# Kernel tuning notes

Measured on AMD Instinct MI355X. Metric: run time of the kernel, lower is better.

The kernel has to match this reference:

```python
import jax, jax.numpy as jnp
import numpy as np

B, C, H, W = 32, 3, 224, 224
P = 14            # n_patches per side
PS = H // P       # 16
D = 768           # embed_size
NH = 12           # heads
DH = D // NH      # 64
L = 12            # n_blocks
FF = 4 * D
OUT = 1000
S = P * P + 1     # 197 tokens


def positional_encoding(seq_len, d):
    i = jnp.arange(seq_len, dtype=jnp.float32)[:, None]
    j = jnp.arange(d, dtype=jnp.float32)[None, :]
    je = jnp.where(j % 2 == 0, j, j - 1)
    ang = i / jnp.power(10000.0, je / d)
    return jnp.where(j % 2 == 0, jnp.sin(ang), jnp.cos(ang))


def layernorm(x, g, b, eps=1e-5):
    mu = jnp.mean(x, axis=-1, keepdims=True)
    var = jnp.var(x, axis=-1, keepdims=True)
    return (x - mu) * jax.lax.rsqrt(var + eps) * g + b


def setup_inputs() -> dict:
    key = jax.random.key(0)
    ks = jax.random.split(key, 20)
    s = 0.02
    inp = {
        'images': jax.random.normal(ks[0], (B, C, H, W), jnp.float32),
        'W_patch': jax.random.normal(ks[1], (D, C * PS * PS), jnp.float32) * s,
        'b_patch': jnp.zeros((D,), jnp.float32),
        'class_token': jax.random.uniform(ks[2], (1, D), jnp.float32),
        'ln1_g': jnp.ones((L, D), jnp.float32),
        'ln1_b': jnp.zeros((L, D), jnp.float32),
        'Wq': jax.random.normal(ks[3], (L, NH, DH, DH), jnp.float32) * s,
        'bq': jnp.zeros((L, NH, DH), jnp.float32),
        'Wk': jax.random.normal(ks[4], (L, NH, DH, DH), jnp.float32) * s,
        'bk': jnp.zeros((L, NH, DH), jnp.float32),
        'Wv': jax.random.normal(ks[5], (L, NH, DH, DH), jnp.float32) * s,
        'bv': jnp.zeros((L, NH, DH), jnp.float32),
        'ln2_g': jnp.ones((L, D), jnp.float32),
        'ln2_b': jnp.zeros((L, D), jnp.float32),
        'W1': jax.random.normal(ks[6], (L, FF, D), jnp.float32) * s,
        'b1': jnp.zeros((L, FF), jnp.float32),
        'W2': jax.random.normal(ks[7], (L, D, FF), jnp.float32) * s,
        'b2': jnp.zeros((L, D), jnp.float32),
        'Wo': jax.random.normal(ks[8], (OUT, D), jnp.float32) * s,
        'bo': jnp.zeros((OUT,), jnp.float32),
    }
    return inp


def reference(images, W_patch, b_patch, class_token, ln1_g, ln1_b,
              Wq, bq, Wk, bk, Wv, bv, ln2_g, ln2_b, W1, b1, W2, b2, Wo, bo):
    b = images.shape[0]
    # patch extraction: [B,C,P,ps,P,ps] -> [B,P*P, C*ps*ps] (flatten order C,h,w)
    patches = images.reshape(b, C, P, PS, P, PS).transpose(0, 2, 4, 1, 3, 5)
    patches = patches.reshape(b, P * P, C * PS * PS)
    tokens = patches @ W_patch.T + b_patch                     # [B, P^2, D]
    cls = jnp.broadcast_to(class_token[None], (b, 1, D))
    x = jnp.concatenate([cls, tokens], axis=1)                 # [B, S, D]
    x = x + positional_encoding(S, D)

    scale = 1.0 / jnp.sqrt(jnp.float32(DH))
    for l in range(L):
        h = layernorm(x, ln1_g[l], ln1_b[l])
        hh = h.reshape(b, S, NH, DH)
        q = jnp.einsum('bshd,hed->bshe', hh, Wq[l]) + bq[l]
        k = jnp.einsum('bshd,hed->bshe', hh, Wk[l]) + bk[l]
        v = jnp.einsum('bshd,hed->bshe', hh, Wv[l]) + bv[l]
        scores = jnp.einsum('bshe,bthe->bhst', q, k) * scale   # [B,H,S,S]
        attn = jax.nn.softmax(scores, axis=-1)
        o = jnp.einsum('bhst,bthe->bshe', attn, v).reshape(b, S, D)
        x = x + o
        h2 = layernorm(x, ln2_g[l], ln2_b[l])
        ff = jax.nn.gelu(h2 @ W1[l].T + b1[l], approximate=False) @ W2[l].T + b2[l]
        x = x + ff

    logits = x[:, 0] @ Wo.T + bo                               # [B, OUT]
    return jax.nn.softmax(logits, axis=-1)
```

## Files before the change

### kernel.cpp

```cpp
#include <hip/hip_runtime.h>
#include <math.h>

static constexpr int kB   = 32;
static constexpr int kC   = 3;
static constexpr int kH   = 224;
static constexpr int kW   = 224;
static constexpr int kP   = 14;
static constexpr int kPS  = 16;
static constexpr int kD   = 768;
static constexpr int kNH  = 12;
static constexpr int kDH  = 64;
static constexpr int kL   = 12;
static constexpr int kFF  = 3072;
static constexpr int kOUT = 1000;
static constexpr int kS   = 197;
static constexpr int kTOK = kB * kS;
static constexpr int kNP  = kP * kP;
static constexpr int kMP  = 6400;
static constexpr int kQKV = 3 * kD;

typedef unsigned short u16;
typedef __attribute__((ext_vector_type(4))) float f32x4;
typedef __attribute__((ext_vector_type(8))) short bf16x8;

__device__ __forceinline__ u16 f2bf(float x) {
    unsigned u = __float_as_uint(x);
    return (u16)((u + 0x7FFFu + ((u >> 16) & 1u)) >> 16);
}
__device__ __forceinline__ float bf2f(u16 x) {
    return __uint_as_float((unsigned)x << 16);
}
__device__ __forceinline__ void cp16_async(void* lds, const void* g) {
    __builtin_amdgcn_global_load_lds((const __attribute__((address_space(1))) unsigned*)g,
                                     (__attribute__((address_space(3))) unsigned*)lds,
                                     16, 0, 0);
}

__global__ void vit_posenc(float* __restrict__ pos) {
    int idx = blockIdx.x * 256 + threadIdx.x;
    if (idx >= kS * kD) return;
    int s = idx / kD, d = idx % kD;
    int je = d & ~1;
    double p = pow(10000.0, (double)je / (double)kD);
    float ang = (float)((double)s / p);
    pos[idx] = (d & 1) ? cosf(ang) : sinf(ang);
}

__global__ void vit_im2col_bf16(const float* __restrict__ img, u16* __restrict__ patches) {
    long idx = (long)blockIdx.x * 256 + threadIdx.x;
    if (idx >= (long)kMP * kD) return;
    int col = (int)(idx % kD);
    long rp = idx / kD;
    if (rp >= (long)kB * kNP) { patches[idx] = 0; return; }
    int p = (int)(rp % kNP), b = (int)(rp / kNP);
    int c = col >> 8;
    int rem = col & 255;
    int i = rem >> 4, j = rem & 15;
    int py = p / kP, px = p % kP;
    patches[idx] = f2bf(img[(((long)b * kC + c) * kH + py * kPS + i) * kW + px * kPS + j]);
}

__global__ void vit_assemble(const float* __restrict__ tokens, const float* __restrict__ cls,
                             const float* __restrict__ pos, float* __restrict__ x) {
    long idx = (long)blockIdx.x * 256 + threadIdx.x;
    if (idx >= (long)kMP * kD) return;
    int d = (int)(idx % kD);
    long bs = idx / kD;
    if (bs >= kTOK) { x[idx] = 0.0f; return; }
    int s = (int)(bs % kS);
    long b = bs / kS;
    float v = (s == 0) ? cls[d] : tokens[((long)b * kNP + (s - 1)) * kD + d];
    x[idx] = v + pos[s * kD + d];
}

__global__ void cast_bf16(const float* __restrict__ in, u16* __restrict__ out, long n4) {
    long i = (long)blockIdx.x * 256 + threadIdx.x;
    if (i >= n4) return;
    float4 v = *(const float4*)(in + i * 4);
    *(ushort4*)(out + i * 4) = make_ushort4(f2bf(v.x), f2bf(v.y), f2bf(v.z), f2bf(v.w));
}

__global__ void zero_u16(u16* __restrict__ p, long n) {
    long i = (long)blockIdx.x * 256 + threadIdx.x;
    if (i < n) p[i] = 0;
}

__global__ void build_whb(const float* __restrict__ Wq, const float* __restrict__ Wk,
                          const float* __restrict__ Wv, const float* __restrict__ bq,
                          const float* __restrict__ bk, const float* __restrict__ bv,
                          u16* __restrict__ Wh, float* __restrict__ bh) {
    int idx = blockIdx.x * 256 + threadIdx.x;
    if (idx >= kNH * 192 * 64) return;
    int d = idx & 63;
    int r = (idx >> 6) % 192;
    int h = idx / (192 * 64);
    int sec = r >> 6, e = r & 63;
    const float* W = (sec == 0) ? Wq : (sec == 1) ? Wk : Wv;
    Wh[idx] = f2bf(W[((h << 6) + e) * 64 + d]);
    if (d == 0) {
        const float* bs = (sec == 0) ? bq : (sec == 1) ? bk : bv;
        bh[h * 192 + r] = bs[(h << 6) + e];
    }
}

__global__ __launch_bounds__(256) void vit_ln(const float* __restrict__ x,
                                              const float* __restrict__ g,
                                              const float* __restrict__ b,
                                              u16* __restrict__ out) {
    long t = blockIdx.x;
    const float* xr = x + t * kD;
    int tid = threadIdx.x;
    float v0 = xr[tid], v1 = xr[tid + 256], v2 = xr[tid + 512];
    float s  = v0 + v1 + v2;
    float sq = v0 * v0 + v1 * v1 + v2 * v2;
    #pragma unroll
    for (int o = 32; o; o >>= 1) { s += __shfl_xor(s, o); sq += __shfl_xor(sq, o); }
    __shared__ float red[8];
    int wid = tid >> 6, lane = tid & 63;
    if (lane == 0) { red[wid] = s; red[4 + wid] = sq; }
    __syncthreads();
    s  = red[0] + red[1] + red[2] + red[3];
    sq = red[4] + red[5] + red[6] + red[7];
    float mu  = s * (1.0f / kD);
    float var = sq * (1.0f / kD) - mu * mu;
    float rs  = rsqrtf(var + 1e-5f);
    u16* orow = out + t * kD;
    orow[tid]       = f2bf((v0 - mu) * rs * g[tid]       + b[tid]);
    orow[tid + 256] = f2bf((v1 - mu) * rs * g[tid + 256] + b[tid + 256]);
    orow[tid + 512] = f2bf((v2 - mu) * rs * g[tid + 512] + b[tid + 512]);
}

template <int EPI>
__global__ __launch_bounds__(256) void mm_bt(const u16* __restrict__ A, int lda,
                                             const u16* __restrict__ B, int ldb,
                                             const float* __restrict__ bias,
                                             const float* X, void* Cout, int ldc, int K) {
    __shared__ __align__(16) u16 As[3][4096];
    __shared__ __align__(16) u16 Bs[3][4096];

    const int gx = gridDim.x, gy = gridDim.y;
    const int nwg = gx * gy;
    const int disp = blockIdx.y * gx + blockIdx.x;
    const int q8 = nwg >> 3, r8 = nwg & 7;
    const int xcd = disp & 7, lot = disp >> 3;
    const int work = (xcd < r8 ? xcd * (q8 + 1) : r8 * (q8 + 1) + (xcd - r8) * q8) + lot;
    const int row0 = (work / gy) << 7;
    const int col0 = (work % gy) << 7;

    const int tid  = threadIdx.x;
    const int lane = tid & 63;
    const int wm = ((tid >> 6) >> 1) << 6;
    const int wn = ((tid >> 6) & 1) << 6;
    const int lr = lane & 15, lhi = lane >> 4;

    const int srow = tid >> 2;
    const int sch  = (((tid & 3) ^ ((srow >> 1) & 3)) << 3);
    const u16* Ag = A + (long)(row0 + srow) * lda + sch;
    const u16* Bg = B + (long)(col0 + srow) * ldb + sch;
    const long Astep = 64L * lda, Bstep = 64L * ldb;
    const int ldst = tid << 3;

    f32x4 acc[4][4] = {};
    const int nk = K >> 5;

    auto stage = [&](int buf, int k0) {
        cp16_async(&As[buf][ldst],        Ag + k0);
        cp16_async(&As[buf][ldst + 2048], Ag + Astep + k0);
        cp16_async(&Bs[buf][ldst],        Bg + k0);
        cp16_async(&Bs[buf][ldst + 2048], Bg + Bstep + k0);
    };
    stage(0, 0);
    stage(1, 32);

    const int rch = (lhi ^ ((lr >> 1) & 3)) << 3;
    int cur = 0;
    for (int t = 0; t < nk; t++) {
        if (t + 1 < nk) asm volatile("s_waitcnt vmcnt(4)" ::: "memory");
        else            asm volatile("s_waitcnt vmcnt(0)" ::: "memory");
        __builtin_amdgcn_sched_barrier(0);
        __builtin_amdgcn_s_barrier();
        bf16x8 af[4], bfr[4];
        #pragma unroll
        for (int m = 0; m < 4; m++)
            af[m] = *(const bf16x8*)&As[cur][(wm + (m << 4) + lr) * 32 + rch];
        #pragma unroll
        for (int n = 0; n < 4; n++)
            bfr[n] = *(const bf16x8*)&Bs[cur][(wn + (n << 4) + lr) * 32 + rch];
        if (t + 2 < nk) {
            int nb = cur + 2; if (nb >= 3) nb -= 3;
            stage(nb, (t + 2) << 5);
        }
        #pragma unroll
        for (int m = 0; m < 4; m++)
            #pragma unroll
            for (int n = 0; n < 4; n++)
                acc[m][n] = __builtin_amdgcn_mfma_f32_16x16x32_bf16(af[m], bfr[n], acc[m][n], 0, 0, 0);
        __builtin_amdgcn_s_barrier();
        cur = (cur + 1 == 3) ? 0 : cur + 1;
    }

    const int r0 = wm + (lhi << 2);
    const int cb = wn + lr;
    #pragma unroll
    for (int n = 0; n < 4; n++) {
        const int cc = col0 + cb + (n << 4);
        const float bv = bias[cc];
        #pragma unroll
        for (int m = 0; m < 4; m++) {
            #pragma unroll
            for (int r = 0; r < 4; r++) {
                const long idx = (long)(row0 + r0 + (m << 4) + r) * ldc + cc;
                float v = acc[m][n][r] + bv;
                if (EPI == 1) {
                    v = 0.5f * v * (1.0f + erff(v * 0.70710678118654752f));
                    ((u16*)Cout)[idx] = f2bf(v);
                } else if (EPI == 2) {
                    ((float*)Cout)[idx] = v + X[idx];
                } else if (EPI == 3) {
                    ((u16*)Cout)[idx] = f2bf(v);
                } else {
                    ((float*)Cout)[idx] = v;
                }
            }
        }
    }
}

__global__ __launch_bounds__(256) void mm_qkv(const u16* __restrict__ hbm,
                                              const u16* __restrict__ Wh,
                                              const float* __restrict__ bh,
                                              u16* __restrict__ qkv) {
    const int h = blockIdx.y;
    const int row0 = blockIdx.x << 6;
    const int tid = threadIdx.x, lane = tid & 63, wave = tid >> 6;
    const int l15 = lane & 15, lhi = lane >> 4;
    const u16* Ab = hbm + h * kDH + (lhi << 3);
    const u16* Bb = Wh + (long)h * 192 * 64 + (lhi << 3);

    bf16x8 af[4][2];
    #pragma unroll
    for (int m = 0; m < 4; m++) {
        const u16* ap = Ab + (long)(row0 + (m << 4) + l15) * kD;
        af[m][0] = *(const bf16x8*)ap;
        af[m][1] = *(const bf16x8*)(ap + 32);
    }
    bf16x8 bfr[3][2];
    #pragma unroll
    for (int n = 0; n < 3; n++) {
        const u16* bp = Bb + (long)(wave * 48 + (n << 4) + l15) * 64;
        bfr[n][0] = *(const bf16x8*)bp;
        bfr[n][1] = *(const bf16x8*)(bp + 32);
    }
    f32x4 acc[4][3] = {};
    __builtin_amdgcn_s_setprio(1);
    #pragma unroll
    for (int m = 0; m < 4; m++)
        #pragma unroll
        for (int n = 0; n < 3; n++) {
            acc[m][n] = __builtin_amdgcn_mfma_f32_16x16x32_bf16(af[m][0], bfr[n][0], acc[m][n], 0, 0, 0);
            acc[m][n] = __builtin_amdgcn_mfma_f32_16x16x32_bf16(af[m][1], bfr[n][1], acc[m][n], 0, 0, 0);
        }
    __builtin_amdgcn_s_setprio(0);
    #pragma unroll
    for (int n = 0; n < 3; n++) {
        const int c = wave * 48 + (n << 4) + l15;
        const int sec = c >> 6, e = c & 63;
        const float bv = bh[h * 192 + c];
        const long gcol = (long)sec * kD + h * kDH + e;
        #pragma unroll
        for (int m = 0; m < 4; m++)
            #pragma unroll
            for (int i = 0; i < 4; i++) {
                const int r = row0 + (m << 4) + (lhi << 2) + i;
                qkv[(long)r * kQKV + gcol] = f2bf(acc[m][n][i] + bv);
            }
    }
}

__global__ __launch_bounds__(256) void vit_attn_fused(const u16* __restrict__ qkv,
                                                      float* __restrict__ x) {
    constexpr int SP = 224;
    constexpr int NT = 13;
    constexpr int LDP = 232;
    __shared__ u16 Plds[64][LDP];
    __shared__ u16 Vt[64][LDP];

    const int z = blockIdx.y, qt = blockIdx.x;
    const int b = z / kNH, h = z % kNH;
    const u16* base = qkv + (long)b * kS * kQKV;
    const u16* Qg = base + h * kDH;
    const u16* Kg = base + kD + h * kDH;
    const u16* Vg = base + 2 * kD + h * kDH;
    const int tid = threadIdx.x, lane = tid & 63, wave = tid >> 6;
    const int l15 = lane & 15, lhi = lane >> 4;

    for (int i = tid; i < (SP * kDH) / 4; i += 256) {
        int s  = i >> 4;
        int d0 = (i & 15) << 2;
        ushort4 v = *(const ushort4*)(Vg + (long)s * kQKV + d0);
        Vt[d0 + 0][s] = v.x; Vt[d0 + 1][s] = v.y;
        Vt[d0 + 2][s] = v.z; Vt[d0 + 3][s] = v.w;
    }

    const int qrow = (qt << 6) + (wave << 4) + l15;
    const u16* qrp = Qg + (long)qrow * kQKV + (lhi << 3);
    const bf16x8 qf0 = *(const bf16x8*)(qrp);
    const bf16x8 qf1 = *(const bf16x8*)(qrp + 32);

    f32x4 sc[NT];
    const u16* krp = Kg + (long)l15 * kQKV + (lhi << 3);
    __builtin_amdgcn_s_setprio(1);
    #pragma unroll
    for (int t = 0; t < NT; t++) {
        const u16* kp = krp + (long)(t << 4) * kQKV;
        bf16x8 kb0 = *(const bf16x8*)(kp);
        bf16x8 kb1 = *(const bf16x8*)(kp + 32);
        f32x4 a = {0.0f, 0.0f, 0.0f, 0.0f};
        a = __builtin_amdgcn_mfma_f32_16x16x32_bf16(qf0, kb0, a, 0, 0, 0);
        a = __builtin_amdgcn_mfma_f32_16x16x32_bf16(qf1, kb1, a, 0, 0, 0);
        sc[t] = a;
    }
    __builtin_amdgcn_s_setprio(0);

    float mx[4] = {-1e30f, -1e30f, -1e30f, -1e30f};
    #pragma unroll
    for (int t = 0; t < NT; t++) {
        const int c = (t << 4) + l15;
        #pragma unroll
        for (int q = 0; q < 4; q++) {
            float v = (c < kS) ? sc[t][q] * 0.125f : -1e30f;
            sc[t][q] = v;
            mx[q] = fmaxf(mx[q], v);
        }
    }
    #pragma unroll
    for (int o = 1; o < 16; o <<= 1)
        #pragma unroll
        for (int q = 0; q < 4; q++) mx[q] = fmaxf(mx[q], __shfl_xor(mx[q], o));
    float sum[4] = {0.0f, 0.0f, 0.0f, 0.0f};
    #pragma unroll
    for (int t = 0; t < NT; t++)
        #pragma unroll
        for (int q = 0; q < 4; q++) {
            float e = __expf(sc[t][q] - mx[q]);
            sc[t][q] = e;
            sum[q] += e;
        }
    #pragma unroll
    for (int o = 1; o < 16; o <<= 1)
        #pragma unroll
        for (int q = 0; q < 4; q++) sum[q] += __shfl_xor(sum[q], o);

    const int prow = (wave << 4) + (lhi << 2);
    #pragma unroll
    for (int t = 0; t < NT; t++)
        #pragma unroll
        for (int q = 0; q < 4; q++)
            Plds[prow + q][(t << 4) + l15] = f2bf(sc[t][q]);
    #pragma unroll
    for (int q = 0; q < 4; q++)
        Plds[prow + q][208 + l15] = 0;
    __syncthreads();

    f32x4 oacc[4] = {};
    const int arow = (wave << 4) + l15;
    const int koff = lhi << 3;
    __builtin_amdgcn_s_setprio(1);
    #pragma unroll
    for (int ks = 0; ks < 7; ks++) {
        bf16x8 pa = *(const bf16x8*)&Plds[arow][ks * 32 + koff];
        #pragma unroll
        for (int n = 0; n < 4; n++) {
            bf16x8 vb = *(const bf16x8*)&Vt[(n << 4) + l15][ks * 32 + koff];
            oacc[n] = __builtin_amdgcn_mfma_f32_16x16x32_bf16(pa, vb, oacc[n], 0, 0, 0);
        }
    }
    __builtin_amdgcn_s_setprio(0);

    const int orow0 = (qt << 6) + (wave << 4) + (lhi << 2);
    #pragma unroll
    for (int q = 0; q < 4; q++) {
        const int r = orow0 + q;
        if (r >= kS) continue;
        const float rinv = 1.0f / sum[q];
        float* xp = x + ((long)b * kS + r) * kD + h * kDH + l15;
        #pragma unroll
        for (int n = 0; n < 4; n++)
            xp[n << 4] += oacc[n][q] * rinv;
    }
}

template <int ACT, int RES>
__global__ __launch_bounds__(256) void vit_gemm(const float* __restrict__ A, long lda, long sAz,
                                                const float* __restrict__ B, long ldb, long sBz,
                                                const float* __restrict__ bias, long sbz,
                                                const float* __restrict__ R,
                                                float* __restrict__ C, long ldc, long sCz,
                                                int M, int N, int K) {
    __shared__ __align__(16) float As[16][64];
    __shared__ __align__(16) float Bs[16][64];
    long z = blockIdx.z;
    A += z * sAz;  B += z * sBz;  C += z * sCz;
    if (bias) bias += z * sbz;
    const float* Rp = nullptr;
    if (RES) Rp = R + z * sCz;

    int row0 = blockIdx.x * 64, col0 = blockIdx.y * 64;
    int tid = threadIdx.x;
    int lr = tid >> 2, lk = (tid & 3) << 2;
    int tm = tid >> 4, tn = tid & 15;
    float acc[4][4] = {};

    for (int k0 = 0; k0 < K; k0 += 16) {
        float4 a = {0, 0, 0, 0}, bb = {0, 0, 0, 0};
        int gr = row0 + lr;
        if (gr < M) a = *(const float4*)(A + (long)gr * lda + k0 + lk);
        int gc = col0 + lr;
        if (gc < N) bb = *(const float4*)(B + (long)gc * ldb + k0 + lk);
        __syncthreads();
        As[lk + 0][lr] = a.x;  As[lk + 1][lr] = a.y;  As[lk + 2][lr] = a.z;  As[lk + 3][lr] = a.w;
        Bs[lk + 0][lr] = bb.x; Bs[lk + 1][lr] = bb.y; Bs[lk + 2][lr] = bb.z; Bs[lk + 3][lr] = bb.w;
        __syncthreads();
        #pragma unroll
        for (int k = 0; k < 16; k++) {
            const float4 av = *reinterpret_cast<const float4*>(&As[k][tm << 2]);
            const float4 bv = *reinterpret_cast<const float4*>(&Bs[k][tn << 2]);
            float aa[4] = {av.x, av.y, av.z, av.w};
            float bw[4] = {bv.x, bv.y, bv.z, bv.w};
            #pragma unroll
            for (int i = 0; i < 4; i++)
                #pragma unroll
                for (int j = 0; j < 4; j++)
                    acc[i][j] = fmaf(aa[i], bw[j], acc[i][j]);
        }
    }
    #pragma unroll
    for (int i = 0; i < 4; i++) {
        int r = row0 + (tm << 2) + i;
        if (r >= M) continue;
        #pragma unroll
        for (int j = 0; j < 4; j++) {
            int c = col0 + (tn << 2) + j;
            if (c >= N) continue;
            float v = acc[i][j];
            if (bias) v += bias[c];
            if (ACT == 1) v = 0.5f * v * (1.0f + erff(v * 0.70710678118654752f));
            if (RES) v += Rp[(long)r * ldc + c];
            C[(long)r * ldc + c] = v;
        }
    }
}

__global__ __launch_bounds__(256) void vit_smout(const float* __restrict__ logits,
                                                 float* __restrict__ out) {
    int b = blockIdx.x;
    const float* p = logits + (long)b * kOUT;
    int tid = threadIdx.x;
    float v[4];
    float mx = -1e30f;
    #pragma unroll
    for (int i = 0; i < 4; i++) {
        int c = tid + (i << 8);
        v[i] = (c < kOUT) ? p[c] : -1e30f;
        mx = fmaxf(mx, v[i]);
    }
    #pragma unroll
    for (int o = 32; o; o >>= 1) mx = fmaxf(mx, __shfl_xor(mx, o));
    __shared__ float red[8];
    int wid = tid >> 6, lane = tid & 63;
    if (lane == 0) red[wid] = mx;
    __syncthreads();
    mx = fmaxf(fmaxf(red[0], red[1]), fmaxf(red[2], red[3]));
    float sum = 0.0f;
    #pragma unroll
    for (int i = 0; i < 4; i++) {
        int c = tid + (i << 8);
        if (c < kOUT) { v[i] = expf(v[i] - mx); sum += v[i]; }
    }
    #pragma unroll
    for (int o = 32; o; o >>= 1) sum += __shfl_xor(sum, o);
    __syncthreads();
    if (lane == 0) red[4 + wid] = sum;
    __syncthreads();
    sum = red[4] + red[5] + red[6] + red[7];
    float inv = 1.0f / sum;
    #pragma unroll
    for (int i = 0; i < 4; i++) {
        int c = tid + (i << 8);
        if (c < kOUT) out[(long)b * kOUT + c] = v[i] * inv;
    }
}

extern "C" void kernel_launch(void* const* d_in, const int* in_sizes, int n_in,
                              void* d_out, int out_size, void* d_ws, size_t ws_size,
                              hipStream_t stream) {
    (void)in_sizes; (void)n_in; (void)out_size; (void)ws_size;
    const float* images  = (const float*)d_in[0];
    const float* W_patch = (const float*)d_in[1];
    const float* b_patch = (const float*)d_in[2];
    const float* cls     = (const float*)d_in[3];
    const float* ln1_g   = (const float*)d_in[4];
    const float* ln1_b   = (const float*)d_in[5];
    const float* Wq      = (const float*)d_in[6];
    const float* bq      = (const float*)d_in[7];
    const float* Wk      = (const float*)d_in[8];
    const float* bk      = (const float*)d_in[9];
    const float* Wv      = (const float*)d_in[10];
    const float* bv      = (const float*)d_in[11];
    const float* ln2_g   = (const float*)d_in[12];
    const float* ln2_b   = (const float*)d_in[13];
    const float* W1      = (const float*)d_in[14];
    const float* b1      = (const float*)d_in[15];
    const float* W2      = (const float*)d_in[16];
    const float* b2      = (const float*)d_in[17];
    const float* Wo      = (const float*)d_in[18];
    const float* bo      = (const float*)d_in[19];

    char* wsB = (char*)d_ws;
    auto alloc = [&](size_t bytes) { char* p = wsB; wsB += (bytes + 255) & ~(size_t)255; return p; };
    float* pos    = (float*)alloc((size_t)kS * kD * 4);
    float* x      = (float*)alloc((size_t)kMP * kD * 4);
    u16*   hb     = (u16*)  alloc((size_t)kMP * kD * 2);
    u16*   qkvb   = (u16*)  alloc((size_t)kMP * kQKV * 2);
    u16*   ff1b   = (u16*)  alloc((size_t)kMP * kFF * 2);
    u16*   W1b    = (u16*)  alloc((size_t)kFF * kD * 2);
    u16*   W2b    = (u16*)  alloc((size_t)kFF * kD * 2);
    u16*   Whb    = (u16*)  alloc((size_t)kNH * 192 * 64 * 2);
    u16*   Wpb    = (u16*)  alloc((size_t)kD * kD * 2);
    float* bhb    = (float*)alloc((size_t)kNH * 192 * 4);
    float* logits = (float*)alloc((size_t)kB * kOUT * 4);
    float* tokens   = (float*)qkvb;
    u16*   patchesb = ff1b;

    vit_posenc<<<(kS * kD + 255) / 256, 256, 0, stream>>>(pos);
    vit_im2col_bf16<<<(int)(((long)kMP * kD) / 256), 256, 0, stream>>>(images, patchesb);
    cast_bf16<<<(kD * kD / 4 + 255) / 256, 256, 0, stream>>>(W_patch, Wpb, (long)kD * kD / 4);
    zero_u16<<<(96 * kD + 255) / 256, 256, 0, stream>>>(hb + (long)kTOK * kD, 96L * kD);
    mm_bt<0><<<dim3(kMP / 128, kD / 128), 256, 0, stream>>>(
        patchesb, kD, Wpb, kD, b_patch, nullptr, tokens, kD, kD);
    vit_assemble<<<(int)(((long)kMP * kD) / 256), 256, 0, stream>>>(tokens, cls, pos, x);

    for (int l = 0; l < kL; l++) {
        cast_bf16<<<(kFF * kD / 4 + 255) / 256, 256, 0, stream>>>(
            W1 + (long)l * kFF * kD, W1b, (long)kFF * kD / 4);
        cast_bf16<<<(kFF * kD / 4 + 255) / 256, 256, 0, stream>>>(
            W2 + (long)l * kFF * kD, W2b, (long)kFF * kD / 4);
        build_whb<<<(kNH * 192 * 64 + 255) / 256, 256, 0, stream>>>(
            Wq + (long)l * kNH * kDH * kDH, Wk + (long)l * kNH * kDH * kDH,
            Wv + (long)l * kNH * kDH * kDH, bq + (long)l * kNH * kDH,
            bk + (long)l * kNH * kDH, bv + (long)l * kNH * kDH, Whb, bhb);

        vit_ln<<<kTOK, 256, 0, stream>>>(x, ln1_g + (long)l * kD, ln1_b + (long)l * kD, hb);
        mm_qkv<<<dim3(kMP / 64, kNH), 256, 0, stream>>>(hb, Whb, bhb, qkvb);

        vit_attn_fused<<<dim3(4, kB * kNH), 256, 0, stream>>>(qkvb, x);

        vit_ln<<<kTOK, 256, 0, stream>>>(x, ln2_g + (long)l * kD, ln2_b + (long)l * kD, hb);
        mm_bt<1><<<dim3(kMP / 128, kFF / 128), 256, 0, stream>>>(
            hb, kD, W1b, kD, b1 + (long)l * kFF, nullptr, ff1b, kFF, kD);
        mm_bt<2><<<dim3(kMP / 128, kD / 128), 256, 0, stream>>>(
            ff1b, kFF, W2b, kFF, b2 + (long)l * kD, x, x, kD, kFF);
    }

    vit_gemm<0, 0><<<dim3(1, 16, 1), 256, 0, stream>>>(
        x, (long)kS * kD, 0, Wo, kD, 0, bo, 0, nullptr,
        logits, kOUT, 0, kB, kOUT, kD);
    vit_smout<<<kB, 256, 0, stream>>>(logits, (float*)d_out);
}
```

Before: 2.544 ms.

## Hoist weight casts, drop GEMM trailing barrier, use polynomial erf GELU

Weight conversion for all layers (W1/W2 bf16 casts and QKV head weight packing) moves out of the per-layer loop into single launches when workspace allows, with W1/W2 casts merged into one kernel otherwise. This cuts per-layer launches and small kernels. The GEMM main loop reorders staging ahead of the LDS fragment reads and replaces the trailing barrier with an lgkmcnt wait, relying on the triple buffer to avoid overwrite hazards. GELU's erff is replaced with the Abramowitz-Stegun polynomial approximation, which adds a small error (around 1e-7 absolute on erf).

```diff
diff --git a/kernel.cpp b/kernel.cpp
--- a/kernel.cpp
+++ b/kernel.cpp
@@ -35,6 +35,16 @@
                                      (__attribute__((address_space(3))) unsigned*)lds,
                                      16, 0, 0);
 }
+__device__ __forceinline__ float gelu_f(float v) {
+    float z = v * 0.70710678118654752f;
+    float s = fabsf(z);
+    float t = 1.0f / (1.0f + 0.3275911f * s);
+    float p = t * (0.254829592f + t * (-0.284496736f +
+              t * (1.421413741f + t * (-1.453152027f + t * 1.061405429f))));
+    float e = p * __expf(-s * s);
+    float erfv = (z < 0.0f) ? (e - 1.0f) : (1.0f - e);
+    return 0.5f * v * (1.0f + erfv);
+}
 
 __global__ void vit_posenc(float* __restrict__ pos) {
     int idx = blockIdx.x * 256 + threadIdx.x;
@@ -79,27 +89,37 @@
     float4 v = *(const float4*)(in + i * 4);
     *(ushort4*)(out + i * 4) = make_ushort4(f2bf(v.x), f2bf(v.y), f2bf(v.z), f2bf(v.w));
 }
+__global__ void cast2_bf16(const float* __restrict__ in1, const float* __restrict__ in2,
+                           u16* __restrict__ out1, u16* __restrict__ out2, long n4each) {
+    long i = (long)blockIdx.x * 256 + threadIdx.x;
+    if (i >= 2 * n4each) return;
+    const float* in = (i < n4each) ? in1 : in2;
+    u16* out        = (i < n4each) ? out1 : out2;
+    long j          = (i < n4each) ? i : i - n4each;
+    float4 v = *(const float4*)(in + j * 4);
+    *(ushort4*)(out + j * 4) = make_ushort4(f2bf(v.x), f2bf(v.y), f2bf(v.z), f2bf(v.w));
+}
 
 __global__ void zero_u16(u16* __restrict__ p, long n) {
     long i = (long)blockIdx.x * 256 + threadIdx.x;
     if (i < n) p[i] = 0;
 }
 
-__global__ void build_whb(const float* __restrict__ Wq, const float* __restrict__ Wk,
-                          const float* __restrict__ Wv, const float* __restrict__ bq,
-                          const float* __restrict__ bk, const float* __restrict__ bv,
-                          u16* __restrict__ Wh, float* __restrict__ bh) {
+__global__ void build_whb_all(const float* __restrict__ Wq, const float* __restrict__ Wk,
+                              const float* __restrict__ Wv, const float* __restrict__ bq,
+                              const float* __restrict__ bk, const float* __restrict__ bv,
+                              u16* __restrict__ Wh, float* __restrict__ bh) {
     int idx = blockIdx.x * 256 + threadIdx.x;
-    if (idx >= kNH * 192 * 64) return;
-    int d = idx & 63;
-    int r = (idx >> 6) % 192;
-    int h = idx / (192 * 64);
+    if (idx >= kL * kNH * 192 * 64) return;
+    int d  = idx & 63;
+    int r  = (idx >> 6) % 192;
+    int lh = (idx >> 6) / 192;
     int sec = r >> 6, e = r & 63;
     const float* W = (sec == 0) ? Wq : (sec == 1) ? Wk : Wv;
-    Wh[idx] = f2bf(W[((h << 6) + e) * 64 + d]);
+    Wh[idx] = f2bf(W[((long)lh * 64 + e) * 64 + d]);
     if (d == 0) {
         const float* bs = (sec == 0) ? bq : (sec == 1) ? bk : bv;
-        bh[h * 192 + r] = bs[(h << 6) + e];
+        bh[lh * 192 + r] = bs[lh * 64 + e];
     }
 }
 
@@ -160,9 +180,6 @@
     const long Astep = 64L * lda, Bstep = 64L * ldb;
     const int ldst = tid << 3;
 
-    f32x4 acc[4][4] = {};
-    const int nk = K >> 5;
-
     auto stage = [&](int buf, int k0) {
         cp16_async(&As[buf][ldst],        Ag + k0);
         cp16_async(&As[buf][ldst + 2048], Ag + Astep + k0);
@@ -172,30 +189,33 @@
     stage(0, 0);
     stage(1, 32);
 
+    f32x4 acc[4][4] = {};
+    const int nk = K >> 5;
     const int rch = (lhi ^ ((lr >> 1) & 3)) << 3;
     int cur = 0;
     for (int t = 0; t < nk; t++) {
         if (t + 1 < nk) asm volatile("s_waitcnt vmcnt(4)" ::: "memory");
         else            asm volatile("s_waitcnt vmcnt(0)" ::: "memory");
+        asm volatile("s_waitcnt lgkmcnt(0)" ::: "memory");
         __builtin_amdgcn_sched_barrier(0);
         __builtin_amdgcn_s_barrier();
-        bf16x8 af[4], bfr[4];
-        #pragma unroll
-        for (int m = 0; m < 4; m++)
-            af[m] = *(const bf16x8*)&As[cur][(wm + (m << 4) + lr) * 32 + rch];
-        #pragma unroll
-        for (int n = 0; n < 4; n++)
-            bfr[n] = *(const bf16x8*)&Bs[cur][(wn + (n << 4) + lr) * 32 + rch];
+        __builtin_amdgcn_sched_barrier(0);
         if (t + 2 < nk) {
             int nb = cur + 2; if (nb >= 3) nb -= 3;
             stage(nb, (t + 2) << 5);
         }
+        bf16x8 af[4], bfr[4];
+        #pragma unroll
+        for (int m = 0; m < 4; m++)
+            af[m] = *(const bf16x8*)&As[cur][(wm + (m << 4) + lr) * 32 + rch];
+        #pragma unroll
+        for (int n = 0; n < 4; n++)
+            bfr[n] = *(const bf16x8*)&Bs[cur][(wn + (n << 4) + lr) * 32 + rch];
         #pragma unroll
         for (int m = 0; m < 4; m++)
             #pragma unroll
             for (int n = 0; n < 4; n++)
                 acc[m][n] = __builtin_amdgcn_mfma_f32_16x16x32_bf16(af[m], bfr[n], acc[m][n], 0, 0, 0);
-        __builtin_amdgcn_s_barrier();
         cur = (cur + 1 == 3) ? 0 : cur + 1;
     }
 
@@ -212,8 +232,7 @@
                 const long idx = (long)(row0 + r0 + (m << 4) + r) * ldc + cc;
                 float v = acc[m][n][r] + bv;
                 if (EPI == 1) {
-                    v = 0.5f * v * (1.0f + erff(v * 0.70710678118654752f));
-                    ((u16*)Cout)[idx] = f2bf(v);
+                    ((u16*)Cout)[idx] = f2bf(gelu_f(v));
                 } else if (EPI == 2) {
                     ((float*)Cout)[idx] = v + X[idx];
                 } else if (EPI == 3) {
@@ -444,7 +463,7 @@
             if (c >= N) continue;
             float v = acc[i][j];
             if (bias) v += bias[c];
-            if (ACT == 1) v = 0.5f * v * (1.0f + erff(v * 0.70710678118654752f));
+            if (ACT == 1) v = gelu_f(v);
             if (RES) v += Rp[(long)r * ldc + c];
             C[(long)r * ldc + c] = v;
         }
@@ -494,7 +513,7 @@
 extern "C" void kernel_launch(void* const* d_in, const int* in_sizes, int n_in,
                               void* d_out, int out_size, void* d_ws, size_t ws_size,
                               hipStream_t stream) {
-    (void)in_sizes; (void)n_in; (void)out_size; (void)ws_size;
+    (void)in_sizes; (void)n_in; (void)out_size;
     const float* images  = (const float*)d_in[0];
     const float* W_patch = (const float*)d_in[1];
     const float* b_patch = (const float*)d_in[2];
@@ -523,43 +542,50 @@
     u16*   hb     = (u16*)  alloc((size_t)kMP * kD * 2);
     u16*   qkvb   = (u16*)  alloc((size_t)kMP * kQKV * 2);
     u16*   ff1b   = (u16*)  alloc((size_t)kMP * kFF * 2);
-    u16*   W1b    = (u16*)  alloc((size_t)kFF * kD * 2);
-    u16*   W2b    = (u16*)  alloc((size_t)kFF * kD * 2);
-    u16*   Whb    = (u16*)  alloc((size_t)kNH * 192 * 64 * 2);
+    u16*   Whb    = (u16*)  alloc((size_t)kL * kNH * 192 * 64 * 2);
     u16*   Wpb    = (u16*)  alloc((size_t)kD * kD * 2);
-    float* bhb    = (float*)alloc((size_t)kNH * 192 * 4);
+    float* bhb    = (float*)alloc((size_t)kL * kNH * 192 * 4);
     float* logits = (float*)alloc((size_t)kB * kOUT * 4);
+
+    const size_t perW  = (size_t)kFF * kD;
+    const size_t used  = (size_t)(wsB - (char*)d_ws);
+    const bool   hoist = ws_size >= used + 2 * kL * perW * 2 + (1u << 20);
+    u16* W12b = (u16*)alloc(hoist ? 2 * kL * perW * 2 : 2 * perW * 2);
+
     float* tokens   = (float*)qkvb;
     u16*   patchesb = ff1b;
 
     vit_posenc<<<(kS * kD + 255) / 256, 256, 0, stream>>>(pos);
     vit_im2col_bf16<<<(int)(((long)kMP * kD) / 256), 256, 0, stream>>>(images, patchesb);
     cast_bf16<<<(kD * kD / 4 + 255) / 256, 256, 0, stream>>>(W_patch, Wpb, (long)kD * kD / 4);
+    build_whb_all<<<(kL * kNH * 192 * 64 + 255) / 256, 256, 0, stream>>>(
+        Wq, Wk, Wv, bq, bk, bv, Whb, bhb);
     zero_u16<<<(96 * kD + 255) / 256, 256, 0, stream>>>(hb + (long)kTOK * kD, 96L * kD);
+    if (hoist)
+        cast2_bf16<<<(int)((2 * kL * perW / 4 + 255) / 256), 256, 0, stream>>>(
+            W1, W2, W12b, W12b + kL * perW, (long)kL * perW / 4);
     mm_bt<0><<<dim3(kMP / 128, kD / 128), 256, 0, stream>>>(
         patchesb, kD, Wpb, kD, b_patch, nullptr, tokens, kD, kD);
     vit_assemble<<<(int)(((long)kMP * kD) / 256), 256, 0, stream>>>(tokens, cls, pos, x);
 
     for (int l = 0; l < kL; l++) {
-        cast_bf16<<<(kFF * kD / 4 + 255) / 256, 256, 0, stream>>>(
-            W1 + (long)l * kFF * kD, W1b, (long)kFF * kD / 4);
-        cast_bf16<<<(kFF * kD / 4 + 255) / 256, 256, 0, stream>>>(
-            W2 + (long)l * kFF * kD, W2b, (long)kFF * kD / 4);
-        build_whb<<<(kNH * 192 * 64 + 255) / 256, 256, 0, stream>>>(
-            Wq + (long)l * kNH * kDH * kDH, Wk + (long)l * kNH * kDH * kDH,
-            Wv + (long)l * kNH * kDH * kDH, bq + (long)l * kNH * kDH,
-            bk + (long)l * kNH * kDH, bv + (long)l * kNH * kDH, Whb, bhb);
+        u16* W1l = hoist ? (W12b + (size_t)l * perW)            : W12b;
+        u16* W2l = hoist ? (W12b + (size_t)(kL + l) * perW)     : W12b + perW;
+        if (!hoist)
+            cast2_bf16<<<(int)((2 * perW / 4 + 255) / 256), 256, 0, stream>>>(
+                W1 + (size_t)l * perW, W2 + (size_t)l * perW, W1l, W2l, (long)perW / 4);
 
         vit_ln<<<kTOK, 256, 0, stream>>>(x, ln1_g + (long)l * kD, ln1_b + (long)l * kD, hb);
-        mm_qkv<<<dim3(kMP / 64, kNH), 256, 0, stream>>>(hb, Whb, bhb, qkvb);
+        mm_qkv<<<dim3(kMP / 64, kNH), 256, 0, stream>>>(
+            hb, Whb + (long)l * kNH * 192 * 64, bhb + (long)l * kNH * 192, qkvb);
 
         vit_attn_fused<<<dim3(4, kB * kNH), 256, 0, stream>>>(qkvb, x);
 
         vit_ln<<<kTOK, 256, 0, stream>>>(x, ln2_g + (long)l * kD, ln2_b + (long)l * kD, hb);
         mm_bt<1><<<dim3(kMP / 128, kFF / 128), 256, 0, stream>>>(
-            hb, kD, W1b, kD, b1 + (long)l * kFF, nullptr, ff1b, kFF, kD);
+            hb, kD, W1l, kD, b1 + (long)l * kFF, nullptr, ff1b, kFF, kD);
         mm_bt<2><<<dim3(kMP / 128, kD / 128), 256, 0, stream>>>(
-            ff1b, kFF, W2b, kFF, b2 + (long)l * kD, x, x, kD, kFF);
+            ff1b, kFF, W2l, kFF, b2 + (long)l * kD, x, x, kD, kFF);
     }
 
     vit_gemm<0, 0><<<dim3(1, 16, 1), 256, 0, stream>>>(
```

New measurement: 2.872 ms. +12.9%, slower.
